# Kernel optimization log

Hardware: AMD Instinct MI355X
Metric: run time of the kernel (lower is better)

## Reference

```python
import jax, jax.numpy as jnp
import numpy as np

B, N, Q, Z, C, L = 1, 6, 20000, 4, 128, 4
IMG_H, IMG_W = 256, 704
PC_RANGE = (-50.0, -50.0, -4.0, 50.0, 50.0, 4.0)
NUM_FREQS = 10
EPS = 1e-5
LEVEL_HW = ((64, 176), (32, 88), (16, 44), (8, 22))


def _mlp(x, ws, bs):
    for i, (w, b) in enumerate(zip(ws, bs)):
        x = x @ w + b
        if i < len(ws) - 1:
            x = jax.nn.relu(x)
    return x


def _bilinear(feat_hwc, px, py):
    # feat_hwc: [H, W, C]; px, py: [P] pixel coords. align_corners=False, zero padding.
    H, W, _ = feat_hwc.shape
    x0 = jnp.floor(px).astype(jnp.int32)
    y0 = jnp.floor(py).astype(jnp.int32)
    wx = px - x0
    wy = py - y0

    def gather(yi, xi):
        inb = ((yi >= 0) & (yi < H) & (xi >= 0) & (xi < W)).astype(feat_hwc.dtype)
        return feat_hwc[jnp.clip(yi, 0, H - 1), jnp.clip(xi, 0, W - 1)] * inb[:, None]

    return (gather(y0, x0) * ((1 - wy) * (1 - wx))[:, None]
          + gather(y0, x0 + 1) * ((1 - wy) * wx)[:, None]
          + gather(y0 + 1, x0) * (wy * (1 - wx))[:, None]
          + gather(y0 + 1, x0 + 1) * (wy * wx)[:, None])


def _pointbev_forward(feats, reference_points, lidar2img,
                      pe_w1, pe_b1, pe_w2, pe_b2, wt_w, wt_b, hm_ws, hm_bs):
    pos = jnp.transpose(reference_points, (0, 2, 1, 3))            # [B,Q,Z,3] in [0,1]
    # sinusoidal positional encoding map (normalized=False: coords used as-is)
    freqs = (2.0 ** jnp.arange(NUM_FREQS, dtype=pos.dtype)) * jnp.pi
    ang = pos[..., None] * freqs                                   # [B,Q,Z,3,F]
    pe_in = jnp.concatenate([jnp.sin(ang), jnp.cos(ang)], axis=-1)
    pe_in = pe_in.reshape(pos.shape[:-1] + (3 * 2 * NUM_FREQS,))
    pos_emb = _mlp(pe_in, [pe_w1, pe_w2], [pe_b1, pe_b2])          # [B,Q,Z,C]
    scale_w = jax.nn.softmax(pos_emb @ wt_w + wt_b, axis=-1)       # [B,Q,Z,L]

    # unnormalize to metric lidar coords via pc_range
    lo = jnp.asarray(PC_RANGE[:3], pos.dtype)
    span = jnp.asarray(PC_RANGE[3:], pos.dtype) - lo
    pts4 = jnp.concatenate([pos * span + lo, jnp.ones_like(pos[..., :1])], axis=-1)
    cam = jnp.einsum('bnij,bqzj->bnqzi', lidar2img, pts4)          # [B,N,Q,Z,4]
    homo = cam[..., 2]
    uv = cam[..., :2] / jnp.maximum(homo, EPS)[..., None]
    u = uv[..., 0] / IMG_W
    v = uv[..., 1] / IMG_H
    valid = ((homo > EPS) & (u > 0.0) & (u < 1.0) & (v > 0.0) & (v < 1.0)).astype(pos.dtype)

    sampler = jax.vmap(_bilinear)
    uf = u.reshape(B * N, Q * Z)
    vf = v.reshape(B * N, Q * Z)
    out = jnp.zeros((B, Q, Z, C), pos.dtype)
    for l, feat in enumerate(feats):                               # L=4 fixed levels
        Hl, Wl = feat.shape[2], feat.shape[3]
        s = sampler(feat.reshape(B * N, Hl, Wl, C), uf * Wl - 0.5, vf * Hl - 0.5)
        s = s.reshape(B, N, Q, Z, C) * valid[..., None]            # mask invalid projections
        out = out + s.sum(axis=1) * scale_w[..., l, None]          # sum views, weight level
    out = (out + pos_emb).reshape(B, Q, Z * C)
    return _mlp(out, hm_ws, hm_bs)                                 # [B,Q,C]


def setup_inputs():
    key = jax.random.key(0)
    ks = jax.random.split(key, 32)
    inp = {}
    for l, (h, w) in enumerate(LEVEL_HW):
        inp[f"feat{l}"] = jax.random.normal(ks[l], (B, N, h, w, C), jnp.float32)
    inp["reference_points"] = jax.random.uniform(ks[8], (B, Z, Q, 3), jnp.float32)
    # structured nuScenes-like lidar2img = intrinsics @ extrinsics for a 6-camera ring
    l2i = np.zeros((B, N, 4, 4), np.float32)
    K = np.array([[400.0, 0.0, IMG_W / 2, 0.0],
                  [0.0, 400.0, IMG_H / 2, 0.0],
                  [0.0, 0.0, 1.0, 0.0],
                  [0.0, 0.0, 0.0, 1.0]], np.float32)
    for n in range(N):
        yaw = 2.0 * np.pi * n / N
        cy, sy = np.cos(yaw), np.sin(yaw)
        R = np.array([[-sy, cy, 0.0], [0.0, 0.0, -1.0], [cy, sy, 0.0]], np.float32)
        E = np.eye(4, dtype=np.float32)
        E[:3, :3] = R
        E[:3, 3] = [0.0, 1.5, 0.5]
        l2i[0, n] = K @ E
    inp["lidar2img"] = jnp.asarray(l2i)

    def lin(k, fi, fo):
        s = 1.0 / np.sqrt(fi)
        return jax.random.uniform(k, (fi, fo), jnp.float32, -s, s)

    d_in = 3 * 2 * NUM_FREQS
    inp["pe_w1"] = lin(ks[9], d_in, 2 * C); inp["pe_b1"] = jnp.zeros((2 * C,), jnp.float32)
    inp["pe_w2"] = lin(ks[10], 2 * C, C);   inp["pe_b2"] = jnp.zeros((C,), jnp.float32)
    inp["wt_w"] = lin(ks[11], C, L);        inp["wt_b"] = jnp.zeros((L,), jnp.float32)
    dims = [Z * C, 2 * Z * C, 2 * Z * C, 2 * Z * C, C]
    for i in range(4):
        inp[f"hm_w{i+1}"] = lin(ks[12 + i], dims[i], dims[i + 1])
        inp[f"hm_b{i+1}"] = jnp.zeros((dims[i + 1],), jnp.float32)
    return inp


def reference(feat0, feat1, feat2, feat3, reference_points, lidar2img,
              pe_w1, pe_b1, pe_w2, pe_b2, wt_w, wt_b,
              hm_w1, hm_b1, hm_w2, hm_b2, hm_w3, hm_b3, hm_w4, hm_b4):
    return _pointbev_forward((feat0, feat1, feat2, feat3), reference_points, lidar2img,
                             pe_w1, pe_b1, pe_w2, pe_b2, wt_w, wt_b,
                             [hm_w1, hm_w2, hm_w3, hm_w4], [hm_b1, hm_b2, hm_b3, hm_b4])
```

## Files before the change

### kernel.cpp

```cpp
#include <hip/hip_runtime.h>
#include <math.h>

#define QN 20000
#define PN 80000
#define CN 128
#define NVIEW 6

typedef __attribute__((ext_vector_type(8))) _Float16 h8;
typedef __attribute__((ext_vector_type(4))) _Float16 h4;
typedef __attribute__((ext_vector_type(4))) float f32x4;

__device__ __forceinline__ void gload16(const void* g, void* l) {
  __builtin_amdgcn_global_load_lds(
      (const __attribute__((address_space(1))) void*)g,
      (__attribute__((address_space(3))) void*)l, 16, 0, 0);
}

__global__ __launch_bounds__(256) void wtrans_kernel(const float* __restrict__ W,
                                                     _Float16* __restrict__ T,
                                                     int K, int N, int Kp) {
  __shared__ float t[32][33];
  const int n0 = blockIdx.x * 32, k0 = blockIdx.y * 32;
  const int tx = threadIdx.x & 31, ty = threadIdx.x >> 5;
  #pragma unroll
  for (int j = 0; j < 4; ++j) {
    int k = k0 + ty + j * 8;
    t[ty + j * 8][tx] = (k < K) ? W[(size_t)k * N + n0 + tx] : 0.f;
  }
  __syncthreads();
  #pragma unroll
  for (int j = 0; j < 4; ++j) {
    int n = n0 + ty + j * 8;
    int k = k0 + tx;
    T[(size_t)n * Kp + k] = (_Float16)t[tx][ty + j * 8];
  }
}

__global__ __launch_bounds__(256) void pe_in_kernel(const float* __restrict__ rp,
                                                    _Float16* __restrict__ P) {
  int idx = blockIdx.x * 256 + threadIdx.x;
  if (idx >= PN * 64) return;
  int p = idx >> 6, k = idx & 63;
  float val = 0.f;
  if (k < 60) {
    int q = p >> 2, z = p & 3;
    int d = k / 20, r = k - d * 20;
    int j = (r >= 10) ? (r - 10) : r;
    float pos = rp[((size_t)z * QN + q) * 3 + d];
    float ang = pos * ((float)(1 << j) * 3.14159265358979323846f);
    val = (r >= 10) ? cosf(ang) : sinf(ang);
  }
  P[idx] = (_Float16)val;
}

template <bool RELU, int OUT>
__global__ __launch_bounds__(256, 4) void gemm_h(const _Float16* __restrict__ A,
                                                 const _Float16* __restrict__ B,
                                                 const float* __restrict__ bias,
                                                 float* __restrict__ Cf,
                                                 _Float16* __restrict__ Ch,
                                                 int M, int N, int K,
                                                 int nbn, int nks) {
  __shared__ _Float16 sm[2][2][4096];
  const int tid = threadIdx.x;
  const int wave = tid >> 6, lane = tid & 63;
  const int wr = wave >> 1, wc = wave & 1;
  const int g = lane >> 4, r16 = lane & 15;

  const int nwg = gridDim.x;
  const int q8 = nwg >> 3, r8 = nwg & 7;
  const int xcd = blockIdx.x & 7, sub = blockIdx.x >> 3;
  const int wg = (xcd < r8 ? xcd * (q8 + 1) : r8 * (q8 + 1) + (xcd - r8) * q8) + sub;
  const int bn = (wg % nbn) * 128;
  const int rem = wg / nbn;
  const int bm = (rem / nks) * 128;
  const int kc = rem % nks;
  const int kbase = kc * (K / nks);
  const int nt = (K / nks) >> 5;

  f32x4 acc[4][4];
  #pragma unroll
  for (int i = 0; i < 4; ++i)
    #pragma unroll
    for (int j = 0; j < 4; ++j) acc[i][j] = {0.f, 0.f, 0.f, 0.f};

  auto STAGE = [&](int buf, int t) {
    const int kof = kbase + (t << 5);
    const int rsub = lane >> 2;
    const int slot0 = lane & 3;
    #pragma unroll
    for (int pl = 0; pl < 2; ++pl) {
      const _Float16* P = (pl == 0) ? A : B;
      const int rbase = (pl == 0) ? bm : bn;
      #pragma unroll
      for (int i = 0; i < 2; ++i) {
        int group = wave * 2 + i;
        int row = group * 16 + rsub;
        int slot = slot0 ^ ((row >> 1) & 3);
        int gr = rbase + row;
        if (pl == 0 && gr >= M) gr = M - 1;
        gload16(P + (size_t)gr * K + kof + slot * 8,
                &sm[buf][pl][group * 512]);
      }
    }
  };

  auto COMPUTE = [&](int buf) {
    h8 a[4], b[4];
    #pragma unroll
    for (int mi = 0; mi < 4; ++mi) {
      int row = wr * 64 + mi * 16 + r16;
      int off = row * 32 + ((g ^ ((row >> 1) & 3)) * 8);
      a[mi] = *(const h8*)&sm[buf][0][off];
    }
    #pragma unroll
    for (int ni = 0; ni < 4; ++ni) {
      int row = wc * 64 + ni * 16 + r16;
      int off = row * 32 + ((g ^ ((row >> 1) & 3)) * 8);
      b[ni] = *(const h8*)&sm[buf][1][off];
    }
    #pragma unroll
    for (int mi = 0; mi < 4; ++mi)
      #pragma unroll
      for (int ni = 0; ni < 4; ++ni)
        acc[mi][ni] = __builtin_amdgcn_mfma_f32_16x16x32_f16(a[mi], b[ni], acc[mi][ni], 0, 0, 0);
  };

  STAGE(0, 0);
  __syncthreads();

  for (int t = 0; t < nt; ++t) {
    if (t + 1 < nt) STAGE((t + 1) & 1, t + 1);
    COMPUTE(t & 1);
    __syncthreads();
  }

  #pragma unroll
  for (int mi = 0; mi < 4; ++mi) {
    int gr0 = bm + wr * 64 + mi * 16 + (lane >> 4) * 4;
    #pragma unroll
    for (int ni = 0; ni < 4; ++ni) {
      int gc = bn + wc * 64 + ni * 16 + r16;
      float bv = (OUT == 2) ? 0.f : bias[gc];
      #pragma unroll
      for (int r = 0; r < 4; ++r) {
        int row = gr0 + r;
        if (row >= M) continue;
        float v = acc[mi][ni][r] + bv;
        if (RELU) v = fmaxf(v, 0.f);
        if (OUT == 0) {
          Cf[(size_t)row * N + gc] = v;
        } else if (OUT == 2) {
          Cf[(size_t)kc * M * N + (size_t)row * N + gc] = v;
        } else {
          Ch[(size_t)row * N + gc] = (_Float16)v;
        }
      }
    }
  }
}

__global__ __launch_bounds__(256) void kreduce_kernel(const float* __restrict__ part,
                                                      const float* __restrict__ bias,
                                                      float* __restrict__ out) {
  int i = blockIdx.x * 256 + threadIdx.x;
  if (i >= QN * (CN / 4)) return;
  int col4 = (i & 31) * 4;
  const size_t stride = (size_t)QN * CN;
  f32x4 s = *(const f32x4*)(part + (size_t)i * 4);
  s += *(const f32x4*)(part + stride + (size_t)i * 4);
  s += *(const f32x4*)(part + 2 * stride + (size_t)i * 4);
  s += *(const f32x4*)(part + 3 * stride + (size_t)i * 4);
  s += *(const f32x4*)(bias + col4);
  *(f32x4*)(out + (size_t)i * 4) = s;
}

__global__ __launch_bounds__(256) void sample_kernel(
    const float* __restrict__ f0, const float* __restrict__ f1,
    const float* __restrict__ f2, const float* __restrict__ f3,
    const float* __restrict__ rp, const float* __restrict__ l2i,
    const float* __restrict__ wtw, const float* __restrict__ wtb,
    const float* __restrict__ posE, _Float16* __restrict__ X0) {
  __shared__ float sl2i[96];
  __shared__ float swtT[512];
  __shared__ float sb[4];
  const int tid = threadIdx.x;
  if (tid < 96) sl2i[tid] = l2i[tid];
  for (int i = tid; i < 512; i += 256) swtT[(i & 3) * 128 + (i >> 2)] = wtw[i];
  if (tid < 4) sb[tid] = wtb[tid];
  __syncthreads();

  const int wave = tid >> 6, lane = tid & 63;
  const int half = lane >> 5, s = lane & 31;
  const int p = blockIdx.x * 8 + wave * 2 + half;
  const int q = p >> 2, z = p & 3;

  const float X  = rp[((size_t)z * QN + q) * 3 + 0] * 100.f - 50.f;
  const float Y  = rp[((size_t)z * QN + q) * 3 + 1] * 100.f - 50.f;
  const float Zc = rp[((size_t)z * QN + q) * 3 + 2] * 8.f - 4.f;

  const int c0 = s * 4;
  f32x4 pe = *(const f32x4*)(posE + (size_t)p * CN + c0);

  float l0 = pe[0] * swtT[0 * 128 + c0] + pe[1] * swtT[0 * 128 + c0 + 1]
           + pe[2] * swtT[0 * 128 + c0 + 2] + pe[3] * swtT[0 * 128 + c0 + 3];
  float l1 = pe[0] * swtT[1 * 128 + c0] + pe[1] * swtT[1 * 128 + c0 + 1]
           + pe[2] * swtT[1 * 128 + c0 + 2] + pe[3] * swtT[1 * 128 + c0 + 3];
  float l2 = pe[0] * swtT[2 * 128 + c0] + pe[1] * swtT[2 * 128 + c0 + 1]
           + pe[2] * swtT[2 * 128 + c0 + 2] + pe[3] * swtT[2 * 128 + c0 + 3];
  float l3 = pe[0] * swtT[3 * 128 + c0] + pe[1] * swtT[3 * 128 + c0 + 1]
           + pe[2] * swtT[3 * 128 + c0 + 2] + pe[3] * swtT[3 * 128 + c0 + 3];
  #pragma unroll
  for (int off = 16; off > 0; off >>= 1) {
    l0 += __shfl_xor(l0, off);
    l1 += __shfl_xor(l1, off);
    l2 += __shfl_xor(l2, off);
    l3 += __shfl_xor(l3, off);
  }
  l0 += sb[0]; l1 += sb[1]; l2 += sb[2]; l3 += sb[3];
  float mx = fmaxf(fmaxf(l0, l1), fmaxf(l2, l3));
  float ex0 = __expf(l0 - mx), ex1 = __expf(l1 - mx);
  float ex2 = __expf(l2 - mx), ex3 = __expf(l3 - mx);
  float esr = 1.f / (ex0 + ex1 + ex2 + ex3);
  float swl[4] = {ex0 * esr, ex1 * esr, ex2 * esr, ex3 * esr};

  const float* FT[4] = {f0, f1, f2, f3};

  float a0 = 0.f, a1 = 0.f, a2 = 0.f, a3 = 0.f;
  for (int n = 0; n < NVIEW; n++) {
    const float* Mx = sl2i + n * 16;
    float cam0 = Mx[0] * X + Mx[1] * Y + Mx[2]  * Zc + Mx[3];
    float cam1 = Mx[4] * X + Mx[5] * Y + Mx[6]  * Zc + Mx[7];
    float cam2 = Mx[8] * X + Mx[9] * Y + Mx[10] * Zc + Mx[11];
    float denom = fmaxf(cam2, 1e-5f);
    float u = cam0 / denom * (1.f / 704.f);
    float v = cam1 / denom * (1.f / 256.f);
    bool valid = (cam2 > 1e-5f) & (u > 0.f) & (u < 1.f) & (v > 0.f) & (v < 1.f);
    if (valid) {
      #pragma unroll
      for (int l = 0; l < 4; l++) {
        const int Hl = 64 >> l, Wl = 176 >> l;
        float pxl = u * (float)Wl - 0.5f;
        float pyl = v * (float)Hl - 0.5f;
        float fx = floorf(pxl), fy = floorf(pyl);
        int x0 = (int)fx, y0 = (int)fy;
        float wx = pxl - fx, wy = pyl - fy;
        const float wxs[2] = {1.f - wx, wx};
        const float wys[2] = {1.f - wy, wy};
        const float* fb = FT[l] + (size_t)n * (Hl * Wl * CN);
        #pragma unroll
        for (int cy = 0; cy < 2; cy++) {
          #pragma unroll
          for (int cx = 0; cx < 2; cx++) {
            int xi = x0 + cx, yi = y0 + cy;
            bool inb = ((unsigned)xi < (unsigned)Wl) & ((unsigned)yi < (unsigned)Hl);
            int off = inb ? (yi * Wl + xi) * CN : 0;
            float wgt = inb ? (wys[cy] * wxs[cx] * swl[l]) : 0.f;
            f32x4 vv = *(const f32x4*)(fb + off + c0);
            a0 = fmaf(wgt, vv[0], a0);
            a1 = fmaf(wgt, vv[1], a1);
            a2 = fmaf(wgt, vv[2], a2);
            a3 = fmaf(wgt, vv[3], a3);
          }
        }
      }
    }
  }
  h4 o;
  o[0] = (_Float16)(a0 + pe[0]);
  o[1] = (_Float16)(a1 + pe[1]);
  o[2] = (_Float16)(a2 + pe[2]);
  o[3] = (_Float16)(a3 + pe[3]);
  *(h4*)&X0[(size_t)p * CN + c0] = o;
}

extern "C" void kernel_launch(void* const* d_in, const int* in_sizes, int n_in,
                              void* d_out, int out_size, void* d_ws, size_t ws_size,
                              hipStream_t stream) {
  const float* feat0 = (const float*)d_in[0];
  const float* feat1 = (const float*)d_in[1];
  const float* feat2 = (const float*)d_in[2];
  const float* feat3 = (const float*)d_in[3];
  const float* rp    = (const float*)d_in[4];
  const float* l2i   = (const float*)d_in[5];
  const float* pe_w1 = (const float*)d_in[6];
  const float* pe_b1 = (const float*)d_in[7];
  const float* pe_w2 = (const float*)d_in[8];
  const float* pe_b2 = (const float*)d_in[9];
  const float* wt_w  = (const float*)d_in[10];
  const float* wt_b  = (const float*)d_in[11];
  const float* hm_w1 = (const float*)d_in[12];
  const float* hm_b1 = (const float*)d_in[13];
  const float* hm_w2 = (const float*)d_in[14];
  const float* hm_b2 = (const float*)d_in[15];
  const float* hm_w3 = (const float*)d_in[16];
  const float* hm_b3 = (const float*)d_in[17];
  const float* hm_w4 = (const float*)d_in[18];
  const float* hm_b4 = (const float*)d_in[19];
  float* out = (float*)d_out;

  char* ws = (char*)d_ws;
  typedef _Float16 h16;
  h16* wPE1 = (h16*)(ws + 0);
  h16* wPE2 = (h16*)(ws + 65536);
  h16* wH1  = (h16*)(ws + 196608);
  h16* wH2  = (h16*)(ws + 2293760);
  h16* wH3  = (h16*)(ws + 6488064);
  h16* wH4  = (h16*)(ws + 10682368);

  float* posE = (float*)(ws + 11534336);
  h16*   hpe  = (h16*)(ws + 53000192);
  h16*   pein = (h16*)(ws + 94000128);
  h16*   X0   = (h16*)(ws + 53000192);
  h16*   H1   = (h16*)(ws + 94000128);
  h16*   H2   = (h16*)(ws + 11534336);
  h16*   H3   = (h16*)(ws + 94000128);
  float* part = (float*)(ws + 11534336);

  wtrans_kernel<<<dim3(8, 2),   256, 0, stream>>>(pe_w1, wPE1, 60,   256,  64);
  wtrans_kernel<<<dim3(4, 8),   256, 0, stream>>>(pe_w2, wPE2, 256,  128,  256);
  wtrans_kernel<<<dim3(32, 16), 256, 0, stream>>>(hm_w1, wH1,  512,  1024, 512);
  wtrans_kernel<<<dim3(32, 32), 256, 0, stream>>>(hm_w2, wH2,  1024, 1024, 1024);
  wtrans_kernel<<<dim3(32, 32), 256, 0, stream>>>(hm_w3, wH3,  1024, 1024, 1024);
  wtrans_kernel<<<dim3(4, 32),  256, 0, stream>>>(hm_w4, wH4,  1024, 128,  1024);

  pe_in_kernel<<<(PN * 64 + 255) / 256, 256, 0, stream>>>(rp, pein);

  gemm_h<true, 1><<<2 * 625, 256, 0, stream>>>(pein, wPE1, pe_b1, nullptr, hpe, PN, 256, 64, 2, 1);
  gemm_h<false, 0><<<1 * 625, 256, 0, stream>>>(hpe, wPE2, pe_b2, posE, nullptr, PN, 128, 256, 1, 1);

  sample_kernel<<<PN / 8, 256, 0, stream>>>(feat0, feat1, feat2, feat3, rp, l2i,
                                            wt_w, wt_b, posE, X0);

  gemm_h<true, 1><<<8 * 157, 256, 0, stream>>>(X0, wH1, hm_b1, nullptr, H1, QN, 1024, 512, 8, 1);
  gemm_h<true, 1><<<8 * 157, 256, 0, stream>>>(H1, wH2, hm_b2, nullptr, H2, QN, 1024, 1024, 8, 1);
  gemm_h<true, 1><<<8 * 157, 256, 0, stream>>>(H2, wH3, hm_b3, nullptr, H3, QN, 1024, 1024, 8, 1);
  gemm_h<false, 2><<<4 * 157, 256, 0, stream>>>(H3, wH4, nullptr, part, nullptr, QN, 128, 1024, 1, 4);
  kreduce_kernel<<<(QN * (CN / 4) + 255) / 256, 256, 0, stream>>>(part, hm_b4, out);
}
```

Baseline: 331.2 us.

## Widen GEMM tile to 128x256 and process 8 channels per sample lane

The GEMM tile grows from 128x128 to 128x256. Each wave now owns a full 128-row by 64-column slice, so every A fragment loaded from LDS feeds four MFMAs, and the kernel allows only 2 workgroups per CU because of the larger register and LDS footprint. B rows are clamped to N so the 128-wide layers (PE2 and the last head layer) still work with half-empty tiles. Separately, the sampling kernel gives each lane 8 channels instead of 4, with 16 lanes per point, which halves the number of threads per point and widens the loads and stores. This cuts LDS traffic per MFMA but reduces occupancy and leaves the tile half idle on N=128 layers.

```diff
diff --git a/kernel.cpp b/kernel.cpp
--- a/kernel.cpp
+++ b/kernel.cpp
@@ -54,33 +54,34 @@
 }
 
 template <bool RELU, int OUT>
-__global__ __launch_bounds__(256, 4) void gemm_h(const _Float16* __restrict__ A,
+__global__ __launch_bounds__(256, 2) void gemm_h(const _Float16* __restrict__ A,
                                                  const _Float16* __restrict__ B,
                                                  const float* __restrict__ bias,
                                                  float* __restrict__ Cf,
                                                  _Float16* __restrict__ Ch,
                                                  int M, int N, int K,
                                                  int nbn, int nks) {
-  __shared__ _Float16 sm[2][2][4096];
+  __shared__ _Float16 smA[2][128 * 32];
+  __shared__ _Float16 smB[2][256 * 32];
   const int tid = threadIdx.x;
   const int wave = tid >> 6, lane = tid & 63;
-  const int wr = wave >> 1, wc = wave & 1;
+  const int wc = wave;
   const int g = lane >> 4, r16 = lane & 15;
 
   const int nwg = gridDim.x;
   const int q8 = nwg >> 3, r8 = nwg & 7;
   const int xcd = blockIdx.x & 7, sub = blockIdx.x >> 3;
   const int wg = (xcd < r8 ? xcd * (q8 + 1) : r8 * (q8 + 1) + (xcd - r8) * q8) + sub;
-  const int bn = (wg % nbn) * 128;
+  const int bn = (wg % nbn) * 256;
   const int rem = wg / nbn;
   const int bm = (rem / nks) * 128;
   const int kc = rem % nks;
   const int kbase = kc * (K / nks);
   const int nt = (K / nks) >> 5;
 
-  f32x4 acc[4][4];
-  #pragma unroll
-  for (int i = 0; i < 4; ++i)
+  f32x4 acc[8][4];
+  #pragma unroll
+  for (int i = 0; i < 8; ++i)
     #pragma unroll
     for (int j = 0; j < 4; ++j) acc[i][j] = {0.f, 0.f, 0.f, 0.f};
 
@@ -89,41 +90,40 @@
     const int rsub = lane >> 2;
     const int slot0 = lane & 3;
     #pragma unroll
-    for (int pl = 0; pl < 2; ++pl) {
-      const _Float16* P = (pl == 0) ? A : B;
-      const int rbase = (pl == 0) ? bm : bn;
-      #pragma unroll
-      for (int i = 0; i < 2; ++i) {
-        int group = wave * 2 + i;
-        int row = group * 16 + rsub;
-        int slot = slot0 ^ ((row >> 1) & 3);
-        int gr = rbase + row;
-        if (pl == 0 && gr >= M) gr = M - 1;
-        gload16(P + (size_t)gr * K + kof + slot * 8,
-                &sm[buf][pl][group * 512]);
-      }
+    for (int i = 0; i < 2; ++i) {
+      int group = wave * 2 + i;
+      int row = group * 16 + rsub;
+      int slot = slot0 ^ ((row >> 1) & 3);
+      int gr = bm + row; if (gr >= M) gr = M - 1;
+      gload16(A + (size_t)gr * K + kof + slot * 8, &smA[buf][group * 512]);
+    }
+    #pragma unroll
+    for (int i = 0; i < 4; ++i) {
+      int group = wave * 4 + i;
+      int row = group * 16 + rsub;
+      int slot = slot0 ^ ((row >> 1) & 3);
+      int gr = bn + row; if (gr >= N) gr = N - 1;
+      gload16(B + (size_t)gr * K + kof + slot * 8, &smB[buf][group * 512]);
     }
   };
 
   auto COMPUTE = [&](int buf) {
-    h8 a[4], b[4];
-    #pragma unroll
-    for (int mi = 0; mi < 4; ++mi) {
-      int row = wr * 64 + mi * 16 + r16;
-      int off = row * 32 + ((g ^ ((row >> 1) & 3)) * 8);
-      a[mi] = *(const h8*)&sm[buf][0][off];
-    }
+    h8 b[4];
     #pragma unroll
     for (int ni = 0; ni < 4; ++ni) {
       int row = wc * 64 + ni * 16 + r16;
       int off = row * 32 + ((g ^ ((row >> 1) & 3)) * 8);
-      b[ni] = *(const h8*)&sm[buf][1][off];
-    }
-    #pragma unroll
-    for (int mi = 0; mi < 4; ++mi)
+      b[ni] = *(const h8*)&smB[buf][off];
+    }
+    #pragma unroll
+    for (int mi = 0; mi < 8; ++mi) {
+      int row = mi * 16 + r16;
+      int off = row * 32 + ((g ^ ((row >> 1) & 3)) * 8);
+      h8 a = *(const h8*)&smA[buf][off];
       #pragma unroll
       for (int ni = 0; ni < 4; ++ni)
-        acc[mi][ni] = __builtin_amdgcn_mfma_f32_16x16x32_f16(a[mi], b[ni], acc[mi][ni], 0, 0, 0);
+        acc[mi][ni] = __builtin_amdgcn_mfma_f32_16x16x32_f16(a, b[ni], acc[mi][ni], 0, 0, 0);
+    }
   };
 
   STAGE(0, 0);
@@ -136,11 +136,12 @@
   }
 
   #pragma unroll
-  for (int mi = 0; mi < 4; ++mi) {
-    int gr0 = bm + wr * 64 + mi * 16 + (lane >> 4) * 4;
+  for (int mi = 0; mi < 8; ++mi) {
+    int gr0 = bm + mi * 16 + (lane >> 4) * 4;
     #pragma unroll
     for (int ni = 0; ni < 4; ++ni) {
       int gc = bn + wc * 64 + ni * 16 + r16;
+      if (gc >= N) continue;
       float bv = (OUT == 2) ? 0.f : bias[gc];
       #pragma unroll
       for (int r = 0; r < 4; ++r) {
@@ -191,42 +192,43 @@
   __syncthreads();
 
   const int wave = tid >> 6, lane = tid & 63;
-  const int half = lane >> 5, s = lane & 31;
-  const int p = blockIdx.x * 8 + wave * 2 + half;
+  const int grp = lane >> 4, s = lane & 15;
+  const int p = blockIdx.x * 16 + wave * 4 + grp;
   const int q = p >> 2, z = p & 3;
 
   const float X  = rp[((size_t)z * QN + q) * 3 + 0] * 100.f - 50.f;
   const float Y  = rp[((size_t)z * QN + q) * 3 + 1] * 100.f - 50.f;
   const float Zc = rp[((size_t)z * QN + q) * 3 + 2] * 8.f - 4.f;
 
-  const int c0 = s * 4;
-  f32x4 pe = *(const f32x4*)(posE + (size_t)p * CN + c0);
-
-  float l0 = pe[0] * swtT[0 * 128 + c0] + pe[1] * swtT[0 * 128 + c0 + 1]
-           + pe[2] * swtT[0 * 128 + c0 + 2] + pe[3] * swtT[0 * 128 + c0 + 3];
-  float l1 = pe[0] * swtT[1 * 128 + c0] + pe[1] * swtT[1 * 128 + c0 + 1]
-           + pe[2] * swtT[1 * 128 + c0 + 2] + pe[3] * swtT[1 * 128 + c0 + 3];
-  float l2 = pe[0] * swtT[2 * 128 + c0] + pe[1] * swtT[2 * 128 + c0 + 1]
-           + pe[2] * swtT[2 * 128 + c0 + 2] + pe[3] * swtT[2 * 128 + c0 + 3];
-  float l3 = pe[0] * swtT[3 * 128 + c0] + pe[1] * swtT[3 * 128 + c0 + 1]
-           + pe[2] * swtT[3 * 128 + c0 + 2] + pe[3] * swtT[3 * 128 + c0 + 3];
-  #pragma unroll
-  for (int off = 16; off > 0; off >>= 1) {
-    l0 += __shfl_xor(l0, off);
-    l1 += __shfl_xor(l1, off);
-    l2 += __shfl_xor(l2, off);
-    l3 += __shfl_xor(l3, off);
-  }
-  l0 += sb[0]; l1 += sb[1]; l2 += sb[2]; l3 += sb[3];
-  float mx = fmaxf(fmaxf(l0, l1), fmaxf(l2, l3));
-  float ex0 = __expf(l0 - mx), ex1 = __expf(l1 - mx);
-  float ex2 = __expf(l2 - mx), ex3 = __expf(l3 - mx);
+  const int c0 = s * 8;
+  f32x4 pe0 = *(const f32x4*)(posE + (size_t)p * CN + c0);
+  f32x4 pe1 = *(const f32x4*)(posE + (size_t)p * CN + c0 + 4);
+
+  float lg[4];
+  #pragma unroll
+  for (int l = 0; l < 4; ++l) {
+    const float* w = swtT + l * 128 + c0;
+    lg[l] = pe0[0] * w[0] + pe0[1] * w[1] + pe0[2] * w[2] + pe0[3] * w[3]
+          + pe1[0] * w[4] + pe1[1] * w[5] + pe1[2] * w[6] + pe1[3] * w[7];
+  }
+  #pragma unroll
+  for (int off = 8; off > 0; off >>= 1) {
+    lg[0] += __shfl_xor(lg[0], off);
+    lg[1] += __shfl_xor(lg[1], off);
+    lg[2] += __shfl_xor(lg[2], off);
+    lg[3] += __shfl_xor(lg[3], off);
+  }
+  lg[0] += sb[0]; lg[1] += sb[1]; lg[2] += sb[2]; lg[3] += sb[3];
+  float mx = fmaxf(fmaxf(lg[0], lg[1]), fmaxf(lg[2], lg[3]));
+  float ex0 = __expf(lg[0] - mx), ex1 = __expf(lg[1] - mx);
+  float ex2 = __expf(lg[2] - mx), ex3 = __expf(lg[3] - mx);
   float esr = 1.f / (ex0 + ex1 + ex2 + ex3);
   float swl[4] = {ex0 * esr, ex1 * esr, ex2 * esr, ex3 * esr};
 
   const float* FT[4] = {f0, f1, f2, f3};
 
   float a0 = 0.f, a1 = 0.f, a2 = 0.f, a3 = 0.f;
+  float a4 = 0.f, a5 = 0.f, a6 = 0.f, a7 = 0.f;
   for (int n = 0; n < NVIEW; n++) {
     const float* Mx = sl2i + n * 16;
     float cam0 = Mx[0] * X + Mx[1] * Y + Mx[2]  * Zc + Mx[3];
@@ -256,22 +258,31 @@
             bool inb = ((unsigned)xi < (unsigned)Wl) & ((unsigned)yi < (unsigned)Hl);
             int off = inb ? (yi * Wl + xi) * CN : 0;
             float wgt = inb ? (wys[cy] * wxs[cx] * swl[l]) : 0.f;
-            f32x4 vv = *(const f32x4*)(fb + off + c0);
-            a0 = fmaf(wgt, vv[0], a0);
-            a1 = fmaf(wgt, vv[1], a1);
-            a2 = fmaf(wgt, vv[2], a2);
-            a3 = fmaf(wgt, vv[3], a3);
+            f32x4 v0 = *(const f32x4*)(fb + off + c0);
+            f32x4 v1 = *(const f32x4*)(fb + off + c0 + 4);
+            a0 = fmaf(wgt, v0[0], a0);
+            a1 = fmaf(wgt, v0[1], a1);
+            a2 = fmaf(wgt, v0[2], a2);
+            a3 = fmaf(wgt, v0[3], a3);
+            a4 = fmaf(wgt, v1[0], a4);
+            a5 = fmaf(wgt, v1[1], a5);
+            a6 = fmaf(wgt, v1[2], a6);
+            a7 = fmaf(wgt, v1[3], a7);
           }
         }
       }
     }
   }
-  h4 o;
-  o[0] = (_Float16)(a0 + pe[0]);
-  o[1] = (_Float16)(a1 + pe[1]);
-  o[2] = (_Float16)(a2 + pe[2]);
-  o[3] = (_Float16)(a3 + pe[3]);
-  *(h4*)&X0[(size_t)p * CN + c0] = o;
+  h8 o;
+  o[0] = (_Float16)(a0 + pe0[0]);
+  o[1] = (_Float16)(a1 + pe0[1]);
+  o[2] = (_Float16)(a2 + pe0[2]);
+  o[3] = (_Float16)(a3 + pe0[3]);
+  o[4] = (_Float16)(a4 + pe1[0]);
+  o[5] = (_Float16)(a5 + pe1[1]);
+  o[6] = (_Float16)(a6 + pe1[2]);
+  o[7] = (_Float16)(a7 + pe1[3]);
+  *(h8*)&X0[(size_t)p * CN + c0] = o;
 }
 
 extern "C" void kernel_launch(void* const* d_in, const int* in_sizes, int n_in,
@@ -326,15 +337,15 @@
 
   pe_in_kernel<<<(PN * 64 + 255) / 256, 256, 0, stream>>>(rp, pein);
 
-  gemm_h<true, 1><<<2 * 625, 256, 0, stream>>>(pein, wPE1, pe_b1, nullptr, hpe, PN, 256, 64, 2, 1);
+  gemm_h<true, 1><<<1 * 625, 256, 0, stream>>>(pein, wPE1, pe_b1, nullptr, hpe, PN, 256, 64, 1, 1);
   gemm_h<false, 0><<<1 * 625, 256, 0, stream>>>(hpe, wPE2, pe_b2, posE, nullptr, PN, 128, 256, 1, 1);
 
-  sample_kernel<<<PN / 8, 256, 0, stream>>>(feat0, feat1, feat2, feat3, rp, l2i,
-                                            wt_w, wt_b, posE, X0);
-
-  gemm_h<true, 1><<<8 * 157, 256, 0, stream>>>(X0, wH1, hm_b1, nullptr, H1, QN, 1024, 512, 8, 1);
-  gemm_h<true, 1><<<8 * 157, 256, 0, stream>>>(H1, wH2, hm_b2, nullptr, H2, QN, 1024, 1024, 8, 1);
-  gemm_h<true, 1><<<8 * 157, 256, 0, stream>>>(H2, wH3, hm_b3, nullptr, H3, QN, 1024, 1024, 8, 1);
-  gemm_h<false, 2><<<4 * 157, 256, 0, stream>>>(H3, wH4, nullptr, part, nullptr, QN, 128, 1024, 1, 4);
+  sample_kernel<<<PN / 16, 256, 0, stream>>>(feat0, feat1, feat2, feat3, rp, l2i,
+                                             wt_w, wt_b, posE, X0);
+
+  gemm_h<true, 1><<<4 * 157, 256, 0, stream>>>(X0, wH1, hm_b1, nullptr, H1, QN, 1024, 512, 4, 1);
+  gemm_h<true, 1><<<4 * 157, 256, 0, stream>>>(H1, wH2, hm_b2, nullptr, H2, QN, 1024, 1024, 4, 1);
+  gemm_h<true, 1><<<4 * 157, 256, 0, stream>>>(H2, wH3, hm_b3, nullptr, H3, QN, 1024, 1024, 4, 1);
+  gemm_h<false, 2><<<1 * 157 * 4, 256, 0, stream>>>(H3, wH4, nullptr, part, nullptr, QN, 128, 1024, 1, 4);
   kreduce_kernel<<<(QN * (CN / 4) + 255) / 256, 256, 0, stream>>>(part, hm_b4, out);
 }
```

New measurement: 500.3 us. +51.1%, slower.
